# Optimization experiments

Measured on AMD Instinct MI355X. Metric: run time of the kernel, lower is better.

## Reference

```python
import jax, jax.numpy as jnp
import numpy as np

K = 7            # involution kernel size
GC = 16          # group_channels (fixed in module)
BN_EPS = 1e-5


def setup_inputs() -> dict:
    key = jax.random.key(0)
    ks = jax.random.split(key, 9)
    B, C, H, W = 4, 256, 64, 64
    OUT = 256
    CR = C // 4                     # reduction_ratio = 4
    G = C // GC                     # groups = 16
    x = jax.random.normal(ks[0], (B, C, H, W), dtype=jnp.float32)
    # conv1: 1x1 conv C -> C//4, no bias (followed by BN)
    w1 = jax.random.normal(ks[1], (CR, C), dtype=jnp.float32) * (1.0 / np.sqrt(C))
    gamma = jax.random.uniform(ks[2], (CR,), dtype=jnp.float32, minval=0.5, maxval=1.5)
    beta = jax.random.normal(ks[3], (CR,), dtype=jnp.float32) * 0.1
    mean = jax.random.normal(ks[4], (CR,), dtype=jnp.float32) * 0.1
    var = jax.random.uniform(ks[5], (CR,), dtype=jnp.float32, minval=0.5, maxval=1.5)
    # conv2: 1x1 conv C//4 -> K^2 * groups, with bias
    w2 = jax.random.normal(ks[6], (K * K * G, CR), dtype=jnp.float32) * (1.0 / np.sqrt(CR))
    b2 = jax.random.normal(ks[7], (K * K * G,), dtype=jnp.float32) * 0.01
    # pointwise: 1x1 conv C -> OUT, no bias
    wp = jax.random.normal(ks[8], (OUT, C), dtype=jnp.float32) * (1.0 / np.sqrt(C))
    return {"x": x, "w1": w1, "gamma": gamma, "beta": beta, "mean": mean,
            "var": var, "w2": w2, "b2": b2, "wp": wp}


def reference(x, w1, gamma, beta, mean, var, w2, b2, wp):
    b, c, h, w = x.shape
    groups = c // GC
    # weight-generation branch: 1x1 conv -> BN (inference) -> ReLU -> 1x1 conv
    y = jnp.einsum('oc,bchw->bohw', w1, x)
    scale = (gamma * jax.lax.rsqrt(var + BN_EPS))[None, :, None, None]
    y = jax.nn.relu((y - mean[None, :, None, None]) * scale + beta[None, :, None, None])
    wt = jnp.einsum('oc,bchw->bohw', w2, y) + b2[None, :, None, None]
    wt = wt.reshape(b, groups, 1, K * K, h, w)
    # unfold: (b, c*K*K, h, w) with channel-major ordering (matches torch Unfold)
    p = (K - 1) // 2
    patches = jax.lax.conv_general_dilated_patches(
        x, (K, K), (1, 1), ((p, p), (p, p)))
    patches = patches.reshape(b, groups, GC, K * K, h, w)
    out = (wt * patches).sum(axis=3).reshape(b, c, h, w)
    return jnp.einsum('oc,bchw->bohw', wp, out)
```

## Files before the change

kernel.cpp:

```cpp
#include <hip/hip_runtime.h>

typedef __attribute__((ext_vector_type(8))) short bf16x8;
typedef __attribute__((ext_vector_type(4))) float f32x4;
typedef __attribute__((ext_vector_type(8))) _Float16 h16x8;
typedef unsigned short u16;
typedef unsigned int u32;

__device__ __forceinline__ u16 f2bf(float f) {
    u32 x = __builtin_bit_cast(u32, f);
    return (u16)((x + 0x7fffu + ((x >> 16) & 1u)) >> 16);
}
__device__ __forceinline__ u16 f2h(float f) {
    _Float16 h = (_Float16)f;
    return __builtin_bit_cast(u16, h);
}

__global__ __launch_bounds__(512) void gemm1m_k(
    const float* __restrict__ x,
    const float* __restrict__ w1, const float* __restrict__ gamma,
    const float* __restrict__ beta, const float* __restrict__ mean,
    const float* __restrict__ var,
    u16* __restrict__ ypk)
{
    __shared__ u16 Ws[32 * 64 * 8];
    __shared__ u16 As[2][8 * 64 * 8];
    const int t = threadIdx.x, lane = t & 63, wave = t >> 6;
    const int b = blockIdx.y, n0 = blockIdx.x * 64;
    const int ln = lane & 15, lk = lane >> 4;
    const int wm = wave >> 1, wn = wave & 1;
    const float* xb = x + (size_t)b * 256 * 4096;

    for (int s = t; s < 2048; s += 512) {
        int kg = s >> 6, m = s & 63;
        float sc = gamma[m] * rsqrtf(var[m] + 1e-5f);
        const float4 f0 = *reinterpret_cast<const float4*>(&w1[(size_t)m * 256 + kg * 8]);
        const float4 f1 = *reinterpret_cast<const float4*>(&w1[(size_t)m * 256 + kg * 8 + 4]);
        uint4 v;
        v.x = (u32)f2bf(f0.x * sc) | ((u32)f2bf(f0.y * sc) << 16);
        v.y = (u32)f2bf(f0.z * sc) | ((u32)f2bf(f0.w * sc) << 16);
        v.z = (u32)f2bf(f1.x * sc) | ((u32)f2bf(f1.y * sc) << 16);
        v.w = (u32)f2bf(f1.z * sc) | ((u32)f2bf(f1.w * sc) << 16);
        *reinterpret_cast<uint4*>(&Ws[((kg * 64) + (m ^ (kg & 7))) * 8]) = v;
    }

    const int skg = t >> 6, snn = t & 63;
    float rx[8];
#pragma unroll
    for (int j = 0; j < 8; ++j)
        rx[j] = xb[(size_t)(skg * 8 + j) * 4096 + n0 + snn];
    {
        uint4 v;
        v.x = (u32)f2bf(rx[0]) | ((u32)f2bf(rx[1]) << 16);
        v.y = (u32)f2bf(rx[2]) | ((u32)f2bf(rx[3]) << 16);
        v.z = (u32)f2bf(rx[4]) | ((u32)f2bf(rx[5]) << 16);
        v.w = (u32)f2bf(rx[6]) | ((u32)f2bf(rx[7]) << 16);
        *reinterpret_cast<uint4*>(&As[0][((skg * 64) + (snn ^ skg)) * 8]) = v;
    }
    __syncthreads();

    f32x4 acc[2];
#pragma unroll
    for (int i = 0; i < 2; ++i)
#pragma unroll
        for (int e = 0; e < 4; ++e) acc[i][e] = 0.f;

    for (int ks = 0; ks < 4; ++ks) {
        const int cur = ks & 1;
        if (ks < 3) {
#pragma unroll
            for (int j = 0; j < 8; ++j)
                rx[j] = xb[(size_t)((ks + 1) * 64 + skg * 8 + j) * 4096 + n0 + snn];
        }
#pragma unroll
        for (int k32 = 0; k32 < 2; ++k32) {
            const int kgl = k32 * 4 + lk;
            const int kgw = ks * 8 + kgl;
            bf16x8 a[2];
#pragma unroll
            for (int i = 0; i < 2; ++i) {
                int n = wn * 32 + i * 16 + ln;
                a[i] = *reinterpret_cast<const bf16x8*>(
                    &As[cur][((kgl * 64) + (n ^ kgl)) * 8]);
            }
            const int m = wm * 16 + ln;
            const bf16x8 bfr = *reinterpret_cast<const bf16x8*>(
                &Ws[((kgw * 64) + (m ^ (kgw & 7))) * 8]);
#pragma unroll
            for (int i = 0; i < 2; ++i)
                acc[i] = __builtin_amdgcn_mfma_f32_16x16x32_bf16(a[i], bfr, acc[i], 0, 0, 0);
        }
        if (ks < 3) {
            uint4 v;
            v.x = (u32)f2bf(rx[0]) | ((u32)f2bf(rx[1]) << 16);
            v.y = (u32)f2bf(rx[2]) | ((u32)f2bf(rx[3]) << 16);
            v.z = (u32)f2bf(rx[4]) | ((u32)f2bf(rx[5]) << 16);
            v.w = (u32)f2bf(rx[6]) | ((u32)f2bf(rx[7]) << 16);
            *reinterpret_cast<uint4*>(&As[cur ^ 1][((skg * 64) + (snn ^ skg)) * 8]) = v;
            __syncthreads();
        }
    }

    const int m = wm * 16 + ln;
    const float sc = gamma[m] * rsqrtf(var[m] + 1e-5f);
    const float bv = beta[m] - mean[m] * sc;
    u16* yb = ypk + ((size_t)b * 8 + (m >> 3)) * 4096 * 8 + (m & 7);
#pragma unroll
    for (int i = 0; i < 2; ++i) {
        const int n = n0 + wn * 32 + i * 16 + lk * 4;
#pragma unroll
        for (int r = 0; r < 4; ++r)
            yb[(size_t)(n + r) * 8] = f2bf(fmaxf(acc[i][r] + bv, 0.f));
    }
}

__global__ __launch_bounds__(256, 2) void fusedinv_k(
    const u16* __restrict__ ypk, const float* __restrict__ w2,
    const float* __restrict__ b2, const float* __restrict__ x,
    u16* __restrict__ invpk)
{
    __shared__ alignas(16) char Lds[66560];
    u16* As = (u16*)Lds;
    u16* Ws = (u16*)(Lds + 32768);
    _Float16* xs = (_Float16*)Lds;
    u16* wt16 = (u16*)(Lds + 40960);

    const int t = threadIdx.x, lane = t & 63, wave = t >> 6;
    const int tile = blockIdx.x, g = blockIdx.y, b = blockIdx.z;
    const int ty0 = (tile >> 2) * 16, tx0 = (tile & 3) * 16;
    const int ln = lane & 15, lk = lane >> 4;

    const u16* yb = ypk + (size_t)b * 8 * 4096 * 8;
#pragma unroll
    for (int r = 0; r < 8; ++r) {
        int s = r * 256 + t;
        int kg = s >> 8, n = s & 255;
        int gpix = (ty0 + (n >> 4)) * 64 + tx0 + (n & 15);
        *reinterpret_cast<uint4*>(&As[(size_t)s * 8]) =
            *reinterpret_cast<const uint4*>(&yb[((size_t)kg * 4096 + gpix) * 8]);
    }
#pragma unroll
    for (int r = 0; r < 2; ++r) {
        int s = r * 256 + t;
        int kg = s >> 6, m = s & 63;
        uint4 v = {0u, 0u, 0u, 0u};
        if (m < 49) {
            const float4 f0 = *reinterpret_cast<const float4*>(
                &w2[(size_t)(g * 49 + m) * 64 + kg * 8]);
            const float4 f1 = *reinterpret_cast<const float4*>(
                &w2[(size_t)(g * 49 + m) * 64 + kg * 8 + 4]);
            v.x = (u32)f2bf(f0.x) | ((u32)f2bf(f0.y) << 16);
            v.y = (u32)f2bf(f0.z) | ((u32)f2bf(f0.w) << 16);
            v.z = (u32)f2bf(f1.x) | ((u32)f2bf(f1.y) << 16);
            v.w = (u32)f2bf(f1.z) | ((u32)f2bf(f1.w) << 16);
        }
        *reinterpret_cast<uint4*>(&Ws[(size_t)s * 8]) = v;
    }
    __syncthreads();

    f32x4 acc[16];
#pragma unroll
    for (int i = 0; i < 16; ++i)
#pragma unroll
        for (int e = 0; e < 4; ++e) acc[i][e] = 0.f;

#pragma unroll
    for (int k32 = 0; k32 < 2; ++k32) {
        const int kg = k32 * 4 + lk;
        const bf16x8 wf = *reinterpret_cast<const bf16x8*>(
            &Ws[((kg * 64) + wave * 16 + ln) * 8]);
#pragma unroll
        for (int i = 0; i < 16; ++i) {
            const bf16x8 af = *reinterpret_cast<const bf16x8*>(
                &As[((kg * 256) + i * 16 + ln) * 8]);
            acc[i] = __builtin_amdgcn_mfma_f32_16x16x32_bf16(af, wf, acc[i], 0, 0, 0);
        }
    }
    __syncthreads();

    const int m = wave * 16 + ln;
    if (m < 49) {
        const float bv = b2[g * 49 + m];
#pragma unroll
        for (int i = 0; i < 16; ++i) {
            u16 h0 = f2h(acc[i][0] + bv), h1 = f2h(acc[i][1] + bv);
            u16 h2 = f2h(acc[i][2] + bv), h3 = f2h(acc[i][3] + bv);
            uint2 v;
            v.x = (u32)h0 | ((u32)h1 << 16);
            v.y = (u32)h2 | ((u32)h3 << 16);
            *reinterpret_cast<uint2*>(&wt16[m * 260 + i * 16 + lk * 4]) = v;
        }
    }

    const float* xb = x + (size_t)(b * 256 + g * 16) * 4096;
    for (int idx = t; idx < 968; idx += 256) {
        int plane = idx / 484, sp = idx - plane * 484;
        int sy = sp / 22, sx = sp - sy * 22;
        int gy = ty0 + sy - 3, gx = tx0 + sx - 3;
        uint4 h = {0u, 0u, 0u, 0u};
        if ((unsigned)gy < 64u && (unsigned)gx < 64u) {
            const float* xp = &xb[(size_t)(plane * 8) * 4096 + gy * 64 + gx];
            float f[8];
#pragma unroll
            for (int j = 0; j < 8; ++j) f[j] = xp[(size_t)j * 4096];
            h.x = (u32)f2h(f[0]) | ((u32)f2h(f[1]) << 16);
            h.y = (u32)f2h(f[2]) | ((u32)f2h(f[3]) << 16);
            h.z = (u32)f2h(f[4]) | ((u32)f2h(f[5]) << 16);
            h.w = (u32)f2h(f[6]) | ((u32)f2h(f[7]) << 16);
        }
        *reinterpret_cast<uint4*>(&xs[((size_t)plane * 484 + sp) * 8]) = h;
    }
    __syncthreads();

    const int py = t >> 4, px = t & 15;
    float o[16];
#pragma unroll
    for (int i = 0; i < 16; ++i) o[i] = 0.f;

    for (int dy = 0; dy < 7; ++dy) {
        const int rowb = (py + dy) * 22 + px;
#pragma unroll
        for (int dx = 0; dx < 7; ++dx) {
            const int kk = dy * 7 + dx;
            const float wf = (float)__builtin_bit_cast(_Float16, wt16[kk * 260 + t]);
            const int sp = rowb + dx;
            const h16x8 x0 = *reinterpret_cast<const h16x8*>(&xs[(size_t)sp * 8]);
            const h16x8 x1 = *reinterpret_cast<const h16x8*>(&xs[((size_t)484 + sp) * 8]);
#pragma unroll
            for (int c = 0; c < 8; ++c) {
                o[c]     += wf * (float)x0[c];
                o[8 + c] += wf * (float)x1[c];
            }
        }
    }

    const int pix = (ty0 + py) * 64 + tx0 + px;
#pragma unroll
    for (int h = 0; h < 2; ++h) {
        u16 p[8];
#pragma unroll
        for (int j = 0; j < 8; ++j) p[j] = f2bf(o[h * 8 + j]);
        uint4 v;
        v.x = (u32)p[0] | ((u32)p[1] << 16);
        v.y = (u32)p[2] | ((u32)p[3] << 16);
        v.z = (u32)p[4] | ((u32)p[5] << 16);
        v.w = (u32)p[6] | ((u32)p[7] << 16);
        *reinterpret_cast<uint4*>(
            &invpk[(((size_t)b * 32 + g * 2 + h) * 4096 + pix) * 8]) = v;
    }
}

__global__ __launch_bounds__(256) void mgemm4_k(
    const u16* __restrict__ Apk,
    const float* __restrict__ wp,
    float* __restrict__ Cout)
{
    __shared__ u16 As[2][8 * 128 * 8];
    __shared__ u16 Ws[32 * 64 * 8];

    const int t = threadIdx.x;
    const int lane = t & 63, wave = t >> 6;
    const int m0 = blockIdx.x * 64;
    const int batch = blockIdx.y >> 5;
    const int n0 = (blockIdx.y & 31) * 128;
    const u16* Ab = Apk + (size_t)batch * 32 * 4096 * 8;

    const int n0w = (wave & 1) * 64;
    const int m0w = (wave >> 1) * 32;
    const int ln = lane & 15, lk = lane >> 4;

    for (int s = t; s < 2048; s += 256) {
        int kg = s >> 6, m = s & 63;
        const float4 f0 = *reinterpret_cast<const float4*>(
            &wp[(size_t)(m0 + m) * 256 + kg * 8]);
        const float4 f1 = *reinterpret_cast<const float4*>(
            &wp[(size_t)(m0 + m) * 256 + kg * 8 + 4]);
        uint4 v;
        v.x = (u32)f2bf(f0.x) | ((u32)f2bf(f0.y) << 16);
        v.y = (u32)f2bf(f0.z) | ((u32)f2bf(f0.w) << 16);
        v.z = (u32)f2bf(f1.x) | ((u32)f2bf(f1.y) << 16);
        v.w = (u32)f2bf(f1.z) | ((u32)f2bf(f1.w) << 16);
        *reinterpret_cast<uint4*>(&Ws[((size_t)kg * 64 + (m ^ (kg & 7))) * 8]) = v;
    }

    uint4 rs[4];
#pragma unroll
    for (int r = 0; r < 4; ++r) {
        int s = r * 256 + t, kg = s >> 7, nn = s & 127;
        rs[r] = *reinterpret_cast<const uint4*>(&Ab[((size_t)kg * 4096 + n0 + nn) * 8]);
    }
#pragma unroll
    for (int r = 0; r < 4; ++r) {
        int s = r * 256 + t, kg = s >> 7, nn = s & 127;
        *reinterpret_cast<uint4*>(&As[0][((size_t)kg * 128 + (nn ^ kg)) * 8]) = rs[r];
    }
    __syncthreads();

    f32x4 acc[4][2];
#pragma unroll
    for (int i = 0; i < 4; ++i)
#pragma unroll
        for (int f = 0; f < 2; ++f)
#pragma unroll
            for (int e = 0; e < 4; ++e) acc[i][f][e] = 0.f;

    for (int ks = 0; ks < 4; ++ks) {
        const int cur = ks & 1;
        if (ks < 3) {
#pragma unroll
            for (int r = 0; r < 4; ++r) {
                int s = r * 256 + t, kg = s >> 7, nn = s & 127;
                rs[r] = *reinterpret_cast<const uint4*>(
                    &Ab[(((size_t)(ks + 1) * 8 + kg) * 4096 + n0 + nn) * 8]);
            }
        }
#pragma unroll
        for (int k32 = 0; k32 < 2; ++k32) {
            const int kg = k32 * 4 + lk;
            bf16x8 a[4], bfr[2];
#pragma unroll
            for (int i = 0; i < 4; ++i) {
                int n = n0w + i * 16 + ln;
                a[i] = *reinterpret_cast<const bf16x8*>(
                    &As[cur][((size_t)kg * 128 + (n ^ kg)) * 8]);
            }
            const int kgw = ks * 8 + kg;
#pragma unroll
            for (int f = 0; f < 2; ++f) {
                int m = m0w + f * 16 + ln;
                bfr[f] = *reinterpret_cast<const bf16x8*>(
                    &Ws[((size_t)kgw * 64 + (m ^ (kgw & 7))) * 8]);
            }
#pragma unroll
            for (int i = 0; i < 4; ++i)
#pragma unroll
                for (int f = 0; f < 2; ++f)
                    acc[i][f] = __builtin_amdgcn_mfma_f32_16x16x32_bf16(
                        a[i], bfr[f], acc[i][f], 0, 0, 0);
        }
        if (ks < 3) {
#pragma unroll
            for (int r = 0; r < 4; ++r) {
                int s = r * 256 + t, kg = s >> 7, nn = s & 127;
                *reinterpret_cast<uint4*>(
                    &As[cur ^ 1][((size_t)kg * 128 + (nn ^ kg)) * 8]) = rs[r];
            }
            __syncthreads();
        }
    }

#pragma unroll
    for (int f = 0; f < 2; ++f) {
        const int m = m0 + m0w + f * 16 + ln;
#pragma unroll
        for (int i = 0; i < 4; ++i) {
            const int n = n0 + n0w + i * 16 + lk * 4;
            float4 v = {acc[i][f][0], acc[i][f][1], acc[i][f][2], acc[i][f][3]};
            *reinterpret_cast<float4*>(&Cout[((size_t)batch * 256 + m) * 4096 + n]) = v;
        }
    }
}

extern "C" void kernel_launch(void* const* d_in, const int* in_sizes, int n_in,
                              void* d_out, int out_size, void* d_ws, size_t ws_size,
                              hipStream_t stream)
{
    const float* x     = (const float*)d_in[0];
    const float* w1    = (const float*)d_in[1];
    const float* gamma = (const float*)d_in[2];
    const float* beta  = (const float*)d_in[3];
    const float* mean  = (const float*)d_in[4];
    const float* var   = (const float*)d_in[5];
    const float* w2    = (const float*)d_in[6];
    const float* b2    = (const float*)d_in[7];
    const float* wp    = (const float*)d_in[8];
    float* out = (float*)d_out;

    u16* u = (u16*)d_ws;
    u16* ypk   = u;
    u16* invpk = u + 1048576;

    gemm1m_k<<<dim3(64, 4), 512, 0, stream>>>(x, w1, gamma, beta, mean, var, ypk);
    fusedinv_k<<<dim3(16, 16, 4), 256, 0, stream>>>(ypk, w2, b2, x, invpk);
    mgemm4_k<<<dim3(4, 128), 256, 0, stream>>>(invpk, wp, out);
}
```

Baseline: 50.96 us.

## Double block size in involution and pointwise GEMM kernels, swizzle LDS, vectorize y stores

```diff
diff --git a/kernel.cpp b/kernel.cpp
--- a/kernel.cpp
+++ b/kernel.cpp
@@ -24,6 +24,7 @@
 {
     __shared__ u16 Ws[32 * 64 * 8];
     __shared__ u16 As[2][8 * 64 * 8];
+
     const int t = threadIdx.x, lane = t & 63, wave = t >> 6;
     const int b = blockIdx.y, n0 = blockIdx.x * 64;
     const int ln = lane & 15, lk = lane >> 4;
@@ -75,19 +76,15 @@
         for (int k32 = 0; k32 < 2; ++k32) {
             const int kgl = k32 * 4 + lk;
             const int kgw = ks * 8 + kgl;
-            bf16x8 a[2];
+            const bf16x8 aw = *reinterpret_cast<const bf16x8*>(
+                &Ws[((kgw * 64) + ((wm * 16 + ln) ^ (kgw & 7))) * 8]);
 #pragma unroll
             for (int i = 0; i < 2; ++i) {
-                int n = wn * 32 + i * 16 + ln;
-                a[i] = *reinterpret_cast<const bf16x8*>(
+                const int n = wn * 32 + i * 16 + ln;
+                const bf16x8 bx = *reinterpret_cast<const bf16x8*>(
                     &As[cur][((kgl * 64) + (n ^ kgl)) * 8]);
-            }
-            const int m = wm * 16 + ln;
-            const bf16x8 bfr = *reinterpret_cast<const bf16x8*>(
-                &Ws[((kgw * 64) + (m ^ (kgw & 7))) * 8]);
-#pragma unroll
-            for (int i = 0; i < 2; ++i)
-                acc[i] = __builtin_amdgcn_mfma_f32_16x16x32_bf16(a[i], bfr, acc[i], 0, 0, 0);
+                acc[i] = __builtin_amdgcn_mfma_f32_16x16x32_bf16(aw, bx, acc[i], 0, 0, 0);
+            }
         }
         if (ks < 3) {
             uint4 v;
@@ -100,20 +97,33 @@
         }
     }
 
-    const int m = wm * 16 + ln;
-    const float sc = gamma[m] * rsqrtf(var[m] + 1e-5f);
-    const float bv = beta[m] - mean[m] * sc;
-    u16* yb = ypk + ((size_t)b * 8 + (m >> 3)) * 4096 * 8 + (m & 7);
+    const int mb = wm * 16 + lk * 4;
+    const float4 g4 = *reinterpret_cast<const float4*>(&gamma[mb]);
+    const float4 v4 = *reinterpret_cast<const float4*>(&var[mb]);
+    const float4 be4 = *reinterpret_cast<const float4*>(&beta[mb]);
+    const float4 mn4 = *reinterpret_cast<const float4*>(&mean[mb]);
+    float bv[4];
+    bv[0] = be4.x - mn4.x * (g4.x * rsqrtf(v4.x + 1e-5f));
+    bv[1] = be4.y - mn4.y * (g4.y * rsqrtf(v4.y + 1e-5f));
+    bv[2] = be4.z - mn4.z * (g4.z * rsqrtf(v4.z + 1e-5f));
+    bv[3] = be4.w - mn4.w * (g4.w * rsqrtf(v4.w + 1e-5f));
+    const int kg = mb >> 3, joff = mb & 7;
 #pragma unroll
     for (int i = 0; i < 2; ++i) {
-        const int n = n0 + wn * 32 + i * 16 + lk * 4;
+        const int n = n0 + wn * 32 + i * 16 + ln;
+        u16 p[4];
 #pragma unroll
         for (int r = 0; r < 4; ++r)
-            yb[(size_t)(n + r) * 8] = f2bf(fmaxf(acc[i][r] + bv, 0.f));
-    }
-}
-
-__global__ __launch_bounds__(256, 2) void fusedinv_k(
+            p[r] = f2bf(fmaxf(acc[i][r] + bv[r], 0.f));
+        uint2 v;
+        v.x = (u32)p[0] | ((u32)p[1] << 16);
+        v.y = (u32)p[2] | ((u32)p[3] << 16);
+        *reinterpret_cast<uint2*>(
+            &ypk[(((size_t)b * 8 + kg) * 4096 + n) * 8 + joff]) = v;
+    }
+}
+
+__global__ __launch_bounds__(512, 4) void fusedinv_k(
     const u16* __restrict__ ypk, const float* __restrict__ w2,
     const float* __restrict__ b2, const float* __restrict__ x,
     u16* __restrict__ invpk)
@@ -128,20 +138,19 @@
     const int tile = blockIdx.x, g = blockIdx.y, b = blockIdx.z;
     const int ty0 = (tile >> 2) * 16, tx0 = (tile & 3) * 16;
     const int ln = lane & 15, lk = lane >> 4;
+    const int q = wave >> 1, h = wave & 1;
 
     const u16* yb = ypk + (size_t)b * 8 * 4096 * 8;
 #pragma unroll
-    for (int r = 0; r < 8; ++r) {
-        int s = r * 256 + t;
+    for (int r = 0; r < 4; ++r) {
+        int s = r * 512 + t;
         int kg = s >> 8, n = s & 255;
         int gpix = (ty0 + (n >> 4)) * 64 + tx0 + (n & 15);
-        *reinterpret_cast<uint4*>(&As[(size_t)s * 8]) =
+        *reinterpret_cast<uint4*>(&As[((kg * 256) + (n ^ kg)) * 8]) =
             *reinterpret_cast<const uint4*>(&yb[((size_t)kg * 4096 + gpix) * 8]);
     }
-#pragma unroll
-    for (int r = 0; r < 2; ++r) {
-        int s = r * 256 + t;
-        int kg = s >> 6, m = s & 63;
+    {
+        int kg = t >> 6, m = t & 63;
         uint4 v = {0u, 0u, 0u, 0u};
         if (m < 49) {
             const float4 f0 = *reinterpret_cast<const float4*>(
@@ -153,13 +162,13 @@
             v.z = (u32)f2bf(f1.x) | ((u32)f2bf(f1.y) << 16);
             v.w = (u32)f2bf(f1.z) | ((u32)f2bf(f1.w) << 16);
         }
-        *reinterpret_cast<uint4*>(&Ws[(size_t)s * 8]) = v;
-    }
-    __syncthreads();
-
-    f32x4 acc[16];
-#pragma unroll
-    for (int i = 0; i < 16; ++i)
+        *reinterpret_cast<uint4*>(&Ws[((kg * 64) + (m ^ kg)) * 8]) = v;
+    }
+    __syncthreads();
+
+    f32x4 acc[8];
+#pragma unroll
+    for (int i = 0; i < 8; ++i)
 #pragma unroll
         for (int e = 0; e < 4; ++e) acc[i][e] = 0.f;
 
@@ -167,89 +176,85 @@
     for (int k32 = 0; k32 < 2; ++k32) {
         const int kg = k32 * 4 + lk;
         const bf16x8 wf = *reinterpret_cast<const bf16x8*>(
-            &Ws[((kg * 64) + wave * 16 + ln) * 8]);
-#pragma unroll
-        for (int i = 0; i < 16; ++i) {
+            &Ws[((kg * 64) + ((q * 16 + ln) ^ kg)) * 8]);
+#pragma unroll
+        for (int i = 0; i < 8; ++i) {
+            const int n = (h * 8 + i) * 16 + ln;
             const bf16x8 af = *reinterpret_cast<const bf16x8*>(
-                &As[((kg * 256) + i * 16 + ln) * 8]);
+                &As[((kg * 256) + (n ^ kg)) * 8]);
             acc[i] = __builtin_amdgcn_mfma_f32_16x16x32_bf16(af, wf, acc[i], 0, 0, 0);
         }
     }
     __syncthreads();
 
-    const int m = wave * 16 + ln;
-    if (m < 49) {
-        const float bv = b2[g * 49 + m];
-#pragma unroll
-        for (int i = 0; i < 16; ++i) {
+    const int kk = q * 16 + ln;
+    if (kk < 49) {
+        const float bv = b2[g * 49 + kk];
+#pragma unroll
+        for (int i = 0; i < 8; ++i) {
             u16 h0 = f2h(acc[i][0] + bv), h1 = f2h(acc[i][1] + bv);
             u16 h2 = f2h(acc[i][2] + bv), h3 = f2h(acc[i][3] + bv);
             uint2 v;
             v.x = (u32)h0 | ((u32)h1 << 16);
             v.y = (u32)h2 | ((u32)h3 << 16);
-            *reinterpret_cast<uint2*>(&wt16[m * 260 + i * 16 + lk * 4]) = v;
+            *reinterpret_cast<uint2*>(&wt16[kk * 260 + (h * 8 + i) * 16 + lk * 4]) = v;
         }
     }
 
     const float* xb = x + (size_t)(b * 256 + g * 16) * 4096;
-    for (int idx = t; idx < 968; idx += 256) {
+    for (int idx = t; idx < 968; idx += 512) {
         int plane = idx / 484, sp = idx - plane * 484;
         int sy = sp / 22, sx = sp - sy * 22;
         int gy = ty0 + sy - 3, gx = tx0 + sx - 3;
-        uint4 h = {0u, 0u, 0u, 0u};
+        uint4 hh = {0u, 0u, 0u, 0u};
         if ((unsigned)gy < 64u && (unsigned)gx < 64u) {
             const float* xp = &xb[(size_t)(plane * 8) * 4096 + gy * 64 + gx];
             float f[8];
 #pragma unroll
             for (int j = 0; j < 8; ++j) f[j] = xp[(size_t)j * 4096];
-            h.x = (u32)f2h(f[0]) | ((u32)f2h(f[1]) << 16);
-            h.y = (u32)f2h(f[2]) | ((u32)f2h(f[3]) << 16);
-            h.z = (u32)f2h(f[4]) | ((u32)f2h(f[5]) << 16);
-            h.w = (u32)f2h(f[6]) | ((u32)f2h(f[7]) << 16);
-        }
-        *reinterpret_cast<uint4*>(&xs[((size_t)plane * 484 + sp) * 8]) = h;
-    }
-    __syncthreads();
-
-    const int py = t >> 4, px = t & 15;
-    float o[16];
-#pragma unroll
-    for (int i = 0; i < 16; ++i) o[i] = 0.f;
+            hh.x = (u32)f2h(f[0]) | ((u32)f2h(f[1]) << 16);
+            hh.y = (u32)f2h(f[2]) | ((u32)f2h(f[3]) << 16);
+            hh.z = (u32)f2h(f[4]) | ((u32)f2h(f[5]) << 16);
+            hh.w = (u32)f2h(f[6]) | ((u32)f2h(f[7]) << 16);
+        }
+        *reinterpret_cast<uint4*>(&xs[((size_t)plane * 484 + sp) * 8]) = hh;
+    }
+    __syncthreads();
+
+    const int px = t & 255, half = t >> 8;
+    const int py = px >> 4, pxx = px & 15;
+    float o[8];
+#pragma unroll
+    for (int i = 0; i < 8; ++i) o[i] = 0.f;
 
     for (int dy = 0; dy < 7; ++dy) {
-        const int rowb = (py + dy) * 22 + px;
+        const int rowb = (py + dy) * 22 + pxx;
 #pragma unroll
         for (int dx = 0; dx < 7; ++dx) {
-            const int kk = dy * 7 + dx;
-            const float wf = (float)__builtin_bit_cast(_Float16, wt16[kk * 260 + t]);
-            const int sp = rowb + dx;
-            const h16x8 x0 = *reinterpret_cast<const h16x8*>(&xs[(size_t)sp * 8]);
-            const h16x8 x1 = *reinterpret_cast<const h16x8*>(&xs[((size_t)484 + sp) * 8]);
-#pragma unroll
-            for (int c = 0; c < 8; ++c) {
-                o[c]     += wf * (float)x0[c];
-                o[8 + c] += wf * (float)x1[c];
-            }
-        }
-    }
-
-    const int pix = (ty0 + py) * 64 + tx0 + px;
-#pragma unroll
-    for (int h = 0; h < 2; ++h) {
-        u16 p[8];
-#pragma unroll
-        for (int j = 0; j < 8; ++j) p[j] = f2bf(o[h * 8 + j]);
-        uint4 v;
-        v.x = (u32)p[0] | ((u32)p[1] << 16);
-        v.y = (u32)p[2] | ((u32)p[3] << 16);
-        v.z = (u32)p[4] | ((u32)p[5] << 16);
-        v.w = (u32)p[6] | ((u32)p[7] << 16);
-        *reinterpret_cast<uint4*>(
-            &invpk[(((size_t)b * 32 + g * 2 + h) * 4096 + pix) * 8]) = v;
-    }
-}
-
-__global__ __launch_bounds__(256) void mgemm4_k(
+            const int kkx = dy * 7 + dx;
+            const float wf = (float)__builtin_bit_cast(_Float16, wt16[kkx * 260 + px]);
+            const h16x8 xv = *reinterpret_cast<const h16x8*>(
+                &xs[((size_t)half * 484 + rowb + dx) * 8]);
+#pragma unroll
+            for (int c = 0; c < 8; ++c)
+                o[c] += wf * (float)xv[c];
+        }
+    }
+
+    const int pix = (ty0 + py) * 64 + tx0 + pxx;
+    u16 p[8];
+#pragma unroll
+    for (int j = 0; j < 8; ++j) p[j] = f2bf(o[j]);
+    uint4 v;
+    v.x = (u32)p[0] | ((u32)p[1] << 16);
+    v.y = (u32)p[2] | ((u32)p[3] << 16);
+    v.z = (u32)p[4] | ((u32)p[5] << 16);
+    v.w = (u32)p[6] | ((u32)p[7] << 16);
+    *reinterpret_cast<uint4*>(
+        &invpk[(((size_t)b * 32 + g * 2 + half) * 4096 + pix) * 8]) = v;
+}
+
+__global__ __launch_bounds__(512, 4) void mgemm4_k(
     const u16* __restrict__ Apk,
     const float* __restrict__ wp,
     float* __restrict__ Cout)
@@ -264,11 +269,10 @@
     const int n0 = (blockIdx.y & 31) * 128;
     const u16* Ab = Apk + (size_t)batch * 32 * 4096 * 8;
 
-    const int n0w = (wave & 1) * 64;
-    const int m0w = (wave >> 1) * 32;
+    const int wn = wave & 3, wm = wave >> 2;
     const int ln = lane & 15, lk = lane >> 4;
 
-    for (int s = t; s < 2048; s += 256) {
+    for (int s = t; s < 2048; s += 512) {
         int kg = s >> 6, m = s & 63;
         const float4 f0 = *reinterpret_cast<const float4*>(
             &wp[(size_t)(m0 + m) * 256 + kg * 8]);
@@ -282,22 +286,22 @@
         *reinterpret_cast<uint4*>(&Ws[((size_t)kg * 64 + (m ^ (kg & 7))) * 8]) = v;
     }
 
-    uint4 rs[4];
-#pragma unroll
-    for (int r = 0; r < 4; ++r) {
-        int s = r * 256 + t, kg = s >> 7, nn = s & 127;
+    uint4 rs[2];
+#pragma unroll
+    for (int r = 0; r < 2; ++r) {
+        int s = r * 512 + t, kg = s >> 7, nn = s & 127;
         rs[r] = *reinterpret_cast<const uint4*>(&Ab[((size_t)kg * 4096 + n0 + nn) * 8]);
     }
 #pragma unroll
-    for (int r = 0; r < 4; ++r) {
-        int s = r * 256 + t, kg = s >> 7, nn = s & 127;
+    for (int r = 0; r < 2; ++r) {
+        int s = r * 512 + t, kg = s >> 7, nn = s & 127;
         *reinterpret_cast<uint4*>(&As[0][((size_t)kg * 128 + (nn ^ kg)) * 8]) = rs[r];
     }
     __syncthreads();
 
-    f32x4 acc[4][2];
-#pragma unroll
-    for (int i = 0; i < 4; ++i)
+    f32x4 acc[2][2];
+#pragma unroll
+    for (int i = 0; i < 2; ++i)
 #pragma unroll
         for (int f = 0; f < 2; ++f)
 #pragma unroll
@@ -307,8 +311,8 @@
         const int cur = ks & 1;
         if (ks < 3) {
 #pragma unroll
-            for (int r = 0; r < 4; ++r) {
-                int s = r * 256 + t, kg = s >> 7, nn = s & 127;
+            for (int r = 0; r < 2; ++r) {
+                int s = r * 512 + t, kg = s >> 7, nn = s & 127;
                 rs[r] = *reinterpret_cast<const uint4*>(
                     &Ab[(((size_t)(ks + 1) * 8 + kg) * 4096 + n0 + nn) * 8]);
             }
@@ -316,22 +320,22 @@
 #pragma unroll
         for (int k32 = 0; k32 < 2; ++k32) {
             const int kg = k32 * 4 + lk;
-            bf16x8 a[4], bfr[2];
-#pragma unroll
-            for (int i = 0; i < 4; ++i) {
-                int n = n0w + i * 16 + ln;
+            const int kgw = ks * 8 + kg;
+            bf16x8 a[2], bfr[2];
+#pragma unroll
+            for (int i = 0; i < 2; ++i) {
+                int n = wn * 32 + i * 16 + ln;
                 a[i] = *reinterpret_cast<const bf16x8*>(
                     &As[cur][((size_t)kg * 128 + (n ^ kg)) * 8]);
             }
-            const int kgw = ks * 8 + kg;
 #pragma unroll
             for (int f = 0; f < 2; ++f) {
-                int m = m0w + f * 16 + ln;
+                int m = wm * 32 + f * 16 + ln;
                 bfr[f] = *reinterpret_cast<const bf16x8*>(
                     &Ws[((size_t)kgw * 64 + (m ^ (kgw & 7))) * 8]);
             }
 #pragma unroll
-            for (int i = 0; i < 4; ++i)
+            for (int i = 0; i < 2; ++i)
 #pragma unroll
                 for (int f = 0; f < 2; ++f)
                     acc[i][f] = __builtin_amdgcn_mfma_f32_16x16x32_bf16(
@@ -339,8 +343,8 @@
         }
         if (ks < 3) {
 #pragma unroll
-            for (int r = 0; r < 4; ++r) {
-                int s = r * 256 + t, kg = s >> 7, nn = s & 127;
+            for (int r = 0; r < 2; ++r) {
+                int s = r * 512 + t, kg = s >> 7, nn = s & 127;
                 *reinterpret_cast<uint4*>(
                     &As[cur ^ 1][((size_t)kg * 128 + (nn ^ kg)) * 8]) = rs[r];
             }
@@ -350,10 +354,10 @@
 
 #pragma unroll
     for (int f = 0; f < 2; ++f) {
-        const int m = m0 + m0w + f * 16 + ln;
-#pragma unroll
-        for (int i = 0; i < 4; ++i) {
-            const int n = n0 + n0w + i * 16 + lk * 4;
+        const int m = m0 + wm * 32 + f * 16 + ln;
+#pragma unroll
+        for (int i = 0; i < 2; ++i) {
+            const int n = n0 + wn * 32 + i * 16 + lk * 4;
             float4 v = {acc[i][f][0], acc[i][f][1], acc[i][f][2], acc[i][f][3]};
             *reinterpret_cast<float4*>(&Cout[((size_t)batch * 256 + m) * 4096 + n]) = v;
         }
@@ -380,6 +384,6 @@
     u16* invpk = u + 1048576;
 
     gemm1m_k<<<dim3(64, 4), 512, 0, stream>>>(x, w1, gamma, beta, mean, var, ypk);
-    fusedinv_k<<<dim3(16, 16, 4), 256, 0, stream>>>(ypk, w2, b2, x, invpk);
-    mgemm4_k<<<dim3(4, 128), 256, 0, stream>>>(invpk, wp, out);
-}
+    fusedinv_k<<<dim3(16, 16, 4), 512, 0, stream>>>(ypk, w2, b2, x, invpk);
+    mgemm4_k<<<dim3(4, 128), 512, 0, stream>>>(invpk, wp, out);
+}
```

After: 49.03 us, median of 2. 3.8% less time.
